# Performance work log

Measured on AMD Instinct MI355X. Metric: run time of the kernel, lower is better.

Reference implementation:

```python
import jax, jax.numpy as jnp
from jax import lax
import numpy as np

B, H, W = 16, 512, 512
OPENING_R, EROSION_R, DILATION_R = 5, 2, 1
MIN_SIZE, AREA_THRESHOLD = 2000, 300
INF = np.int32(2 ** 30)


def _disk(r):
    # skimage.morphology.disk: x^2 + y^2 <= r^2 on a (2r+1)^2 grid
    y, x = np.mgrid[-r:r + 1, -r:r + 1]
    return jnp.asarray((x * x + y * y <= r * r).astype(np.float32))


D_OPEN, D_ERODE, D_DILATE = _disk(OPENING_R), _disk(EROSION_R), _disk(DILATION_R)


def _conv2(x, k):
    return lax.conv_general_dilated(x[None, None], k[None, None], (1, 1), 'VALID')[0, 0]


def _erode(fg, se):
    # skimage binary_erosion uses border_value=True (image border does not erode)
    r = se.shape[0] // 2
    x = jnp.pad(fg.astype(jnp.float32), r, constant_values=1.0)
    return _conv2(x, se) >= se.sum() - 0.5


def _dilate(fg, se):
    # skimage binary_dilation uses border_value=False
    r = se.shape[0] // 2
    x = jnp.pad(fg.astype(jnp.float32), r, constant_values=0.0)
    return _conv2(x, se) > 0.5


def _seg_cummin(v, reset, axis, reverse):
    # segmented cumulative-min: scan resets wherever `reset` is True (background)
    def comb(a, b):
        av, af = a
        bv, bf = b
        return jnp.where(bf, bv, jnp.minimum(av, bv)), af | bf

    vv, _ = lax.associative_scan(comb, (v, reset), axis=axis, reverse=reverse)
    return vv


def _label(fg):
    # 4-connectivity connected-component labeling via min-label propagation.
    # Each fg pixel starts with its raveled index; alternating row/col segmented
    # cummin sweeps run under while_loop until a fixed point (root id per comp).
    h, w = fg.shape
    idx = jnp.arange(h * w, dtype=jnp.int32).reshape(h, w)
    lab0 = jnp.where(fg, idx, INF)
    bg = ~fg

    def sweep(l):
        for axis in (1, 0):
            for rev in (False, True):
                l = jnp.where(fg, _seg_cummin(l, bg, axis, rev), INF)
        return l

    def body(c):
        l, _ = c
        nl = sweep(l)
        return nl, jnp.array_equal(nl, l)

    lab, _ = lax.while_loop(lambda c: ~c[1], body, (lab0, jnp.array(False)))
    seg = jnp.where(fg, lab, 0).ravel()
    sizes = jax.ops.segment_sum(fg.astype(jnp.int32).ravel(), seg, num_segments=h * w)
    ncomp = jnp.sum(sizes > 0)
    return lab, sizes, ncomp


def _remove_small_objects(fg, min_size, guard):
    lab, sizes, ncomp = _label(fg)
    px = sizes[jnp.where(fg, lab, 0)]  # component size at every fg pixel
    kept = fg & (px >= min_size)
    # original only removes small objects when label(...).max() > 1
    return jnp.where(ncomp > 1, kept, fg) if guard else kept


def _pipeline(mask):
    fg = mask > 0
    fg = _remove_small_objects(fg, MIN_SIZE, True)
    # remove_small_holes == ~remove_small_objects(~fg, area_threshold + 1)
    fg = ~_remove_small_objects(~fg, AREA_THRESHOLD + 1, False)
    fg = _erode(fg, D_ERODE)
    fg = _dilate(_erode(fg, D_OPEN), D_OPEN)  # binary_opening
    fg = _remove_small_objects(fg, MIN_SIZE, True)
    fg = _dilate(fg, D_DILATE)
    return fg.astype(jnp.float32)  # original casts to int; float32 kept for vjp parity


def setup_inputs() -> dict:
    key = jax.random.key(0)
    # blobby binary masks: threshold bilinearly-upsampled low-res noise so that
    # realistic large connected components (> min_size px) exist
    low = jax.random.uniform(key, (B, H // 16, W // 16), dtype=jnp.float32)
    blob = jax.image.resize(low, (B, H, W), method='bilinear')
    return {'inputs': (blob > 0.5).astype(jnp.float32)}


def reference(inputs):
    return jax.vmap(_pipeline)(inputs)
```

## Files before the change

### kernel.cpp

```cpp
#include <hip/hip_runtime.h>
#include <stdint.h>

#define BATCH 16
#define H 512
#define W 512
#define HW (H * W)
#define NTOT (BATCH * HW)
#define NWORDS (NTOT / 64)

#define TPB 256
#define NBLK ((NTOT + TPB - 1) / TPB)
#define NBLKW ((NWORDS + TPB - 1) / TPB)

#define SROWS 16
#define SWORDS 128
#define SPIX 8192
#define NSTRIPS (NWORDS / SWORDS)

__device__ __forceinline__ int find_root_c(int* L, int x) {
    int r = x, p = L[r];
    while (p != r) { r = p; p = L[r]; }
    if (L[x] != r) atomicMin(&L[x], r);
    return r;
}

__device__ void merge_uf(int* L, int a, int b) {
    while (true) {
        a = find_root_c(L, a);
        b = find_root_c(L, b);
        if (a == b) return;
        int lo = a < b ? a : b;
        int hi = a < b ? b : a;
        int old = atomicMin(&L[hi], lo);
        if (old == hi) return;
        a = lo; b = old;
    }
}

__device__ __forceinline__ int find_root_lds(int* P, int x) {
    int r = x, p = P[r];
    while (p != r) { r = p; p = P[r]; }
    return r;
}

__device__ void merge_lds(int* P, int a, int b) {
    while (true) {
        a = find_root_lds(P, a);
        b = find_root_lds(P, b);
        if (a == b) return;
        int lo = a < b ? a : b;
        int hi = a < b ? b : a;
        int old = atomicMin(&P[hi], lo);
        if (old == hi) return;
        a = lo; b = old;
    }
}

__device__ __forceinline__ int start_of(uint64_t m, int i, int cv, int base) {
    uint64_t below = i ? ((~m) & ((1ull << i) - 1)) : 0ull;
    if (below == 0) return (cv >= 0) ? cv : base;
    int hz = 63 - __builtin_clzll(below);
    return base + hz + 1;
}

__device__ uint64_t fill_word(const uint64_t* __restrict__ bits,
                              const int* __restrict__ carry, const int* __restrict__ L,
                              const int* __restrict__ sizes, int minsz, int gw) {
    uint64_t fg = bits[gw];
    uint64_t bg = ~fg;
    uint64_t res = fg;
    int cv = carry[gw];
    int base = gw << 6;
    while (bg) {
        int s = __builtin_ctzll(bg);
        uint64_t rest = bg >> s;
        uint64_t nr = ~rest;
        int len = nr ? __builtin_ctzll(nr) : (64 - s);
        uint64_t piece = ((len >= 64) ? ~0ull : ((1ull << len) - 1)) << s;
        int start = (s == 0 && cv >= 0) ? cv : (base + s);
        if (sizes[L[start]] < minsz) res |= piece;
        bg &= ~piece;
    }
    return res;
}

template <int R, bool ERODE>
__device__ uint64_t morph_word_lds(const uint64_t* buf, int lrow, int w, int gyTop) {
    const uint64_t BORDER = ERODE ? ~0ull : 0ull;
    uint64_t res = ERODE ? ~0ull : 0ull;
#pragma unroll
    for (int dy = -R; dy <= R; ++dy) {
        int lr = lrow + dy;
        int gy = gyTop + lr;
        if (gy < 0 || gy >= H) continue;
        int v = R * R - dy * dy;
        int kx = 0;
        while ((kx + 1) * (kx + 1) <= v) ++kx;
        uint64_t cur = buf[lr * 8 + w];
        uint64_t prv = (w > 0) ? buf[lr * 8 + w - 1] : BORDER;
        uint64_t nxt = (w < 7) ? buf[lr * 8 + w + 1] : BORDER;
        uint64_t acc = cur;
#pragma unroll
        for (int dx = 1; dx <= kx; ++dx) {
            uint64_t right = (cur >> dx) | (nxt << (64 - dx));
            uint64_t left  = (cur << dx) | (prv >> (64 - dx));
            if (ERODE) acc &= right & left;
            else       acc |= right | left;
        }
        if (ERODE) res &= acc;
        else       res |= acc;
    }
    return res;
}

__global__ void k_thresh_pack(const float* __restrict__ in, uint64_t* __restrict__ bits) {
    int p = blockIdx.x * blockDim.x + threadIdx.x;
    bool a = (p < NTOT) && (in[p] > 0.0f);
    uint64_t b = __ballot(a);
    if ((threadIdx.x & 63) == 0 && p < NTOT) bits[p >> 6] = b;
}

__global__ void k_strip_ccl(const uint64_t* __restrict__ bits, int inv,
                            int* __restrict__ carry, int* __restrict__ L,
                            int* __restrict__ sizes, int* __restrict__ ncomp) {
    __shared__ uint64_t sw[SWORDS];
    __shared__ int scarry[SWORDS];
    __shared__ int par[SPIX];
    int blk = blockIdx.x;
    int t = threadIdx.x;
    uint64_t inv64 = inv ? ~0ull : 0ull;
    uint64_t m = bits[blk * SWORDS + t] ^ inv64;
    sw[t] = m;
    __syncthreads();

    if (t < SROWS) {
        int cv = -1;
        for (int i = 0; i < 8; ++i) {
            int lw = t * 8 + i;
            scarry[lw] = cv;
            uint64_t w = sw[lw];
            if (w >> 63) {
                uint64_t z = ~w;
                if (z == 0) { if (cv < 0) cv = lw << 6; }
                else { int hz = 63 - __builtin_clzll(z); cv = (lw << 6) + hz + 1; }
            } else cv = -1;
        }
    }
    __syncthreads();

    int cv = scarry[t];
    carry[blk * SWORDS + t] = (cv >= 0) ? (blk * SPIX + cv) : -1;
    int lbase = t << 6;
    uint64_t starts = m & ~((m << 1) | ((cv >= 0) ? 1ull : 0ull));
    uint64_t ss = starts;
    while (ss) {
        int s = __builtin_ctzll(ss);
        par[lbase + s] = lbase + s;
        ss &= ss - 1;
    }
    __syncthreads();

    if (t >= 8 && m) {
        uint64_t up = sw[t - 8];
        uint64_t cand = m & up;
        if (cand) {
            uint64_t curprev = (t & 7) ? sw[t - 1] : 0ull;
            uint64_t upprev  = (t & 7) ? sw[t - 9] : 0ull;
            uint64_t curl = (m << 1) | (curprev >> 63);
            uint64_t upl  = (up << 1) | (upprev >> 63);
            cand &= ~(curl & upl);
            int cvu = scarry[t - 8];
            while (cand) {
                int i = __builtin_ctzll(cand);
                int sP = start_of(m, i, cv, lbase);
                int sQ = start_of(up, i, cvu, lbase - 512);
                merge_lds(par, sP, sQ);
                cand &= cand - 1;
            }
        }
    }
    __syncthreads();

    int gpix = blk * SPIX;
    ss = starts;
    while (ss) {
        int s = __builtin_ctzll(ss);
        int ls = lbase + s;
        int r = find_root_lds(par, ls);
        L[gpix + ls] = gpix + r;
        if (r == ls) sizes[gpix + ls] = 0;
        ss &= ss - 1;
    }
    if (t == 0 && (blk & 31) == 0) ncomp[blk >> 5] = 0;
}

__global__ void k_merge_bound(const uint64_t* __restrict__ bits, int inv,
                              const int* __restrict__ carry, int* __restrict__ L) {
    int tid = threadIdx.x;
    if (tid >= 248) return;
    int img = blockIdx.x;
    int y = ((tid >> 3) + 1) * SROWS;
    int w = tid & 7;
    int gw = img * 4096 + y * 8 + w;
    uint64_t inv64 = inv ? ~0ull : 0ull;
    uint64_t cur = bits[gw] ^ inv64;
    uint64_t up  = bits[gw - 8] ^ inv64;
    uint64_t cand = cur & up;
    if (!cand) return;
    uint64_t curprev = w ? (bits[gw - 1] ^ inv64) : 0ull;
    uint64_t upprev  = w ? (bits[gw - 9] ^ inv64) : 0ull;
    uint64_t curl = (cur << 1) | (curprev >> 63);
    uint64_t upl  = (up << 1)  | (upprev >> 63);
    cand &= ~(curl & upl);
    if (!cand) return;
    int cvc = carry[gw], cvu = carry[gw - 8];
    int base = gw << 6;
    while (cand) {
        int i = __builtin_ctzll(cand);
        int sP = start_of(cur, i, cvc, base);
        int sQ = start_of(up, i, cvu, base - W);
        merge_uf(L, sP, sQ);
        cand &= cand - 1;
    }
}

__global__ void k_flatten_count(const uint64_t* __restrict__ bits, int inv,
                                const int* __restrict__ carry, int* __restrict__ L,
                                int* __restrict__ sizes, int* __restrict__ ncomp) {
    __shared__ int hk[128];
    __shared__ int hv[128];
    for (int i = threadIdx.x; i < 128; i += TPB) { hk[i] = -1; hv[i] = 0; }
    __syncthreads();

    int gw = blockIdx.x * blockDim.x + threadIdx.x;
    if (gw < NWORDS) {
        uint64_t inv64 = inv ? ~0ull : 0ull;
        uint64_t m = bits[gw] ^ inv64;
        if (m) {
            int cv = carry[gw];
            int base = gw << 6;
            while (m) {
                int s = __builtin_ctzll(m);
                uint64_t rest = m >> s;
                uint64_t nr = ~rest;
                int len = nr ? __builtin_ctzll(nr) : (64 - s);
                uint64_t piece = ((len >= 64) ? ~0ull : ((1ull << len) - 1)) << s;
                bool initial = !(s == 0 && cv >= 0);
                int start = initial ? (base + s) : cv;
                int r = find_root_c(L, start);
                if (initial && r == start) atomicAdd(&ncomp[gw >> 12], 1);
                int cnt = __popcll(piece);
                uint32_t h = ((uint32_t)r * 2654435761u) >> 25;
                bool done = false;
                for (int tt = 0; tt < 16; ++tt) {
                    int slot = (h + tt) & 127;
                    int k = hk[slot];
                    if (k == -1) k = atomicCAS(&hk[slot], -1, r);
                    if (k == -1 || k == r) { atomicAdd(&hv[slot], cnt); done = true; break; }
                }
                if (!done) atomicAdd(&sizes[r], cnt);
                m &= ~piece;
            }
        }
    }
    __syncthreads();
    for (int i = threadIdx.x; i < 128; i += TPB)
        if (hk[i] != -1) atomicAdd(&sizes[hk[i]], hv[i]);
}

__global__ void k_keep_guard(const uint64_t* __restrict__ bits,
                             const int* __restrict__ carry, const int* __restrict__ L,
                             const int* __restrict__ sizes, const int* __restrict__ ncomp,
                             int minsz, uint64_t* __restrict__ out) {
    int gw = blockIdx.x * blockDim.x + threadIdx.x;
    if (gw >= NWORDS) return;
    uint64_t m = bits[gw];
    uint64_t res = m;
    if (m && ncomp[gw >> 12] > 1) {
        int cv = carry[gw];
        int base = gw << 6;
        while (m) {
            int s = __builtin_ctzll(m);
            uint64_t rest = m >> s;
            uint64_t nr = ~rest;
            int len = nr ? __builtin_ctzll(nr) : (64 - s);
            uint64_t piece = ((len >= 64) ? ~0ull : ((1ull << len) - 1)) << s;
            int start = (s == 0 && cv >= 0) ? cv : (base + s);
            if (sizes[L[start]] < minsz) res &= ~piece;
            m &= ~piece;
        }
    }
    out[gw] = res;
}

__global__ void k_fill_morph(const uint64_t* __restrict__ bits,
                             const int* __restrict__ carry, const int* __restrict__ L,
                             const int* __restrict__ sizes,
                             uint64_t* __restrict__ out) {
    __shared__ uint64_t bufA[56 * 8];
    __shared__ uint64_t bufB[56 * 8];
    int img = blockIdx.x >> 4;
    int s   = blockIdx.x & 15;
    int y0 = s * 32;
    int gyTop = y0 - 12;
    int t = threadIdx.x;

    for (int lw = t; lw < 56 * 8; lw += TPB) {
        int gy = gyTop + (lw >> 3);
        int w = lw & 7;
        uint64_t v = 0;
        if (gy >= 0 && gy < H)
            v = fill_word(bits, carry, L, sizes, 301, img * 4096 + gy * 8 + w);
        bufA[lw] = v;
    }
    __syncthreads();

    for (int lw = t; lw < 56 * 8; lw += TPB) {
        int lr = lw >> 3;
        if (lr < 2 || lr > 53) continue;
        bufB[lw] = morph_word_lds<2, true>(bufA, lr, lw & 7, gyTop);
    }
    __syncthreads();

    for (int lw = t; lw < 56 * 8; lw += TPB) {
        int lr = lw >> 3;
        if (lr < 7 || lr > 48) continue;
        bufA[lw] = morph_word_lds<5, true>(bufB, lr, lw & 7, gyTop);
    }
    __syncthreads();

    for (int lw = t; lw < 56 * 8; lw += TPB) {
        int lr = lw >> 3;
        if (lr < 12 || lr > 43) continue;
        uint64_t v = morph_word_lds<5, false>(bufA, lr, lw & 7, gyTop);
        int gy = gyTop + lr;
        out[img * 4096 + gy * 8 + (lw & 7)] = v;
    }
}

__global__ void k_to_float_dilate(const uint64_t* __restrict__ bits,
                                  float* __restrict__ out) {
    int p = blockIdx.x * blockDim.x + threadIdx.x;
    if (p >= NTOT) return;
    int gw = p >> 6;
    int i = p & 63;
    int w = gw & 7;
    int y = (gw >> 3) & (H - 1);
    uint64_t cur = bits[gw];
    uint64_t up  = (y > 0)     ? bits[gw - 8] : 0ull;
    uint64_t dn  = (y < H - 1) ? bits[gw + 8] : 0ull;
    uint64_t prv = (w > 0)     ? bits[gw - 1] : 0ull;
    uint64_t nxt = (w < 7)     ? bits[gw + 1] : 0ull;
    uint64_t d = cur | up | dn | (cur << 1) | (prv >> 63) | (cur >> 1) | (nxt << 63);
    out[p] = ((d >> i) & 1ull) ? 1.0f : 0.0f;
}

extern "C" void kernel_launch(void* const* d_in, const int* in_sizes, int n_in,
                              void* d_out, int out_size, void* d_ws, size_t ws_size,
                              hipStream_t stream) {
    const float* in = (const float*)d_in[0];
    float* out = (float*)d_out;

    uint8_t* ws = (uint8_t*)d_ws;
    int* labels = (int*)ws;
    int* sizes  = (int*)(ws + (size_t)NTOT * 4);
    uint64_t* bitsA = (uint64_t*)(ws + (size_t)NTOT * 8);
    uint64_t* bitsB = bitsA + NWORDS;
    int* carry = (int*)(bitsB + NWORDS);
    int* ncomp = carry + NWORDS;

    k_thresh_pack<<<NBLK, TPB, 0, stream>>>(in, bitsA);

    k_strip_ccl<<<NSTRIPS, SWORDS, 0, stream>>>(bitsA, 0, carry, labels, sizes, ncomp);
    k_merge_bound<<<BATCH, 256, 0, stream>>>(bitsA, 0, carry, labels);
    k_flatten_count<<<NBLKW, TPB, 0, stream>>>(bitsA, 0, carry, labels, sizes, ncomp);
    k_keep_guard<<<NBLKW, TPB, 0, stream>>>(bitsA, carry, labels, sizes, ncomp, 2000, bitsB);

    k_strip_ccl<<<NSTRIPS, SWORDS, 0, stream>>>(bitsB, 1, carry, labels, sizes, ncomp);
    k_merge_bound<<<BATCH, 256, 0, stream>>>(bitsB, 1, carry, labels);
    k_flatten_count<<<NBLKW, TPB, 0, stream>>>(bitsB, 1, carry, labels, sizes, ncomp);

    k_fill_morph<<<BATCH * 16, TPB, 0, stream>>>(bitsB, carry, labels, sizes, bitsA);

    k_strip_ccl<<<NSTRIPS, SWORDS, 0, stream>>>(bitsA, 0, carry, labels, sizes, ncomp);
    k_merge_bound<<<BATCH, 256, 0, stream>>>(bitsA, 0, carry, labels);
    k_flatten_count<<<NBLKW, TPB, 0, stream>>>(bitsA, 0, carry, labels, sizes, ncomp);
    k_keep_guard<<<NBLKW, TPB, 0, stream>>>(bitsA, carry, labels, sizes, ncomp, 2000, bitsB);

    k_to_float_dilate<<<NBLK, TPB, 0, stream>>>(bitsB, out);
}
```

Measured before the change: 212.6 us.

## Fuse keep-guard into next strip CCL and into final dilate/float output

```diff
diff --git a/kernel.cpp b/kernel.cpp
--- a/kernel.cpp
+++ b/kernel.cpp
@@ -61,6 +61,29 @@
     if (below == 0) return (cv >= 0) ? cv : base;
     int hz = 63 - __builtin_clzll(below);
     return base + hz + 1;
+}
+
+__device__ uint64_t keep_word(const uint64_t* __restrict__ bits,
+                              const int* __restrict__ carry, const int* __restrict__ L,
+                              const int* __restrict__ sizes, const int* __restrict__ ncomp,
+                              int minsz, int gw) {
+    uint64_t m = bits[gw];
+    uint64_t res = m;
+    if (m && ncomp[gw >> 12] > 1) {
+        int cv = carry[gw];
+        int base = gw << 6;
+        while (m) {
+            int s = __builtin_ctzll(m);
+            uint64_t rest = m >> s;
+            uint64_t nr = ~rest;
+            int len = nr ? __builtin_ctzll(nr) : (64 - s);
+            uint64_t piece = ((len >= 64) ? ~0ull : ((1ull << len) - 1)) << s;
+            int start = (s == 0 && cv >= 0) ? cv : (base + s);
+            if (sizes[L[start]] < minsz) res &= ~piece;
+            m &= ~piece;
+        }
+    }
+    return res;
 }
 
 __device__ uint64_t fill_word(const uint64_t* __restrict__ bits,
@@ -113,23 +136,10 @@
     return res;
 }
 
-__global__ void k_thresh_pack(const float* __restrict__ in, uint64_t* __restrict__ bits) {
-    int p = blockIdx.x * blockDim.x + threadIdx.x;
-    bool a = (p < NTOT) && (in[p] > 0.0f);
-    uint64_t b = __ballot(a);
-    if ((threadIdx.x & 63) == 0 && p < NTOT) bits[p >> 6] = b;
-}
-
-__global__ void k_strip_ccl(const uint64_t* __restrict__ bits, int inv,
-                            int* __restrict__ carry, int* __restrict__ L,
-                            int* __restrict__ sizes, int* __restrict__ ncomp) {
-    __shared__ uint64_t sw[SWORDS];
-    __shared__ int scarry[SWORDS];
-    __shared__ int par[SPIX];
-    int blk = blockIdx.x;
-    int t = threadIdx.x;
-    uint64_t inv64 = inv ? ~0ull : 0ull;
-    uint64_t m = bits[blk * SWORDS + t] ^ inv64;
+__device__ void strip_ccl_body(uint64_t m, uint64_t* sw, int* scarry, int* par,
+                               int blk, int t,
+                               int* __restrict__ carry, int* __restrict__ L,
+                               int* __restrict__ sizes, int* __restrict__ ncomp) {
     sw[t] = m;
     __syncthreads();
 
@@ -192,6 +202,43 @@
         ss &= ss - 1;
     }
     if (t == 0 && (blk & 31) == 0) ncomp[blk >> 5] = 0;
+}
+
+__global__ void k_thresh_pack(const float* __restrict__ in, uint64_t* __restrict__ bits) {
+    int p = blockIdx.x * blockDim.x + threadIdx.x;
+    bool a = (p < NTOT) && (in[p] > 0.0f);
+    uint64_t b = __ballot(a);
+    if ((threadIdx.x & 63) == 0 && p < NTOT) bits[p >> 6] = b;
+}
+
+__global__ void k_strip_ccl(const uint64_t* __restrict__ bits, int inv,
+                            int* __restrict__ carry, int* __restrict__ L,
+                            int* __restrict__ sizes, int* __restrict__ ncomp) {
+    __shared__ uint64_t sw[SWORDS];
+    __shared__ int scarry[SWORDS];
+    __shared__ int par[SPIX];
+    int blk = blockIdx.x;
+    int t = threadIdx.x;
+    uint64_t inv64 = inv ? ~0ull : 0ull;
+    uint64_t m = bits[blk * SWORDS + t] ^ inv64;
+    strip_ccl_body(m, sw, scarry, par, blk, t, carry, L, sizes, ncomp);
+}
+
+__global__ void k_keep_strip(const uint64_t* __restrict__ bits,
+                             const int* __restrict__ carryIn, const int* __restrict__ Lin,
+                             const int* __restrict__ sizesIn, const int* __restrict__ ncompIn,
+                             uint64_t* __restrict__ outBits,
+                             int* __restrict__ carryOut, int* __restrict__ Lout,
+                             int* __restrict__ sizesOut, int* __restrict__ ncompOut) {
+    __shared__ uint64_t sw[SWORDS];
+    __shared__ int scarry[SWORDS];
+    __shared__ int par[SPIX];
+    int blk = blockIdx.x;
+    int t = threadIdx.x;
+    int gw = blk * SWORDS + t;
+    uint64_t kw = keep_word(bits, carryIn, Lin, sizesIn, ncompIn, 2000, gw);
+    outBits[gw] = kw;
+    strip_ccl_body(~kw, sw, scarry, par, blk, t, carryOut, Lout, sizesOut, ncompOut);
 }
 
 __global__ void k_merge_bound(const uint64_t* __restrict__ bits, int inv,
@@ -268,31 +315,6 @@
         if (hk[i] != -1) atomicAdd(&sizes[hk[i]], hv[i]);
 }
 
-__global__ void k_keep_guard(const uint64_t* __restrict__ bits,
-                             const int* __restrict__ carry, const int* __restrict__ L,
-                             const int* __restrict__ sizes, const int* __restrict__ ncomp,
-                             int minsz, uint64_t* __restrict__ out) {
-    int gw = blockIdx.x * blockDim.x + threadIdx.x;
-    if (gw >= NWORDS) return;
-    uint64_t m = bits[gw];
-    uint64_t res = m;
-    if (m && ncomp[gw >> 12] > 1) {
-        int cv = carry[gw];
-        int base = gw << 6;
-        while (m) {
-            int s = __builtin_ctzll(m);
-            uint64_t rest = m >> s;
-            uint64_t nr = ~rest;
-            int len = nr ? __builtin_ctzll(nr) : (64 - s);
-            uint64_t piece = ((len >= 64) ? ~0ull : ((1ull << len) - 1)) << s;
-            int start = (s == 0 && cv >= 0) ? cv : (base + s);
-            if (sizes[L[start]] < minsz) res &= ~piece;
-            m &= ~piece;
-        }
-    }
-    out[gw] = res;
-}
-
 __global__ void k_fill_morph(const uint64_t* __restrict__ bits,
                              const int* __restrict__ carry, const int* __restrict__ L,
                              const int* __restrict__ sizes,
@@ -338,21 +360,53 @@
     }
 }
 
-__global__ void k_to_float_dilate(const uint64_t* __restrict__ bits,
-                                  float* __restrict__ out) {
-    int p = blockIdx.x * blockDim.x + threadIdx.x;
-    if (p >= NTOT) return;
-    int gw = p >> 6;
-    int i = p & 63;
-    int w = gw & 7;
-    int y = (gw >> 3) & (H - 1);
-    uint64_t cur = bits[gw];
-    uint64_t up  = (y > 0)     ? bits[gw - 8] : 0ull;
-    uint64_t dn  = (y < H - 1) ? bits[gw + 8] : 0ull;
-    uint64_t prv = (w > 0)     ? bits[gw - 1] : 0ull;
-    uint64_t nxt = (w < 7)     ? bits[gw + 1] : 0ull;
-    uint64_t d = cur | up | dn | (cur << 1) | (prv >> 63) | (cur >> 1) | (nxt << 63);
-    out[p] = ((d >> i) & 1ull) ? 1.0f : 0.0f;
+__global__ void k_keep_dilate_float(const uint64_t* __restrict__ bits,
+                                    const int* __restrict__ carry, const int* __restrict__ L,
+                                    const int* __restrict__ sizes, const int* __restrict__ ncomp,
+                                    float* __restrict__ out) {
+    __shared__ uint64_t kb[10 * 8];
+    __shared__ uint64_t db[8 * 8];
+    int blk = blockIdx.x;
+    int img = blk >> 6;
+    int s = blk & 63;
+    int y0 = s * 8;
+    int t = threadIdx.x;
+
+    if (t < 80) {
+        int lr = t >> 3;
+        int w = t & 7;
+        int gy = y0 - 1 + lr;
+        uint64_t v = 0;
+        if (gy >= 0 && gy < H)
+            v = keep_word(bits, carry, L, sizes, ncomp, 2000, img * 4096 + gy * 8 + w);
+        kb[t] = v;
+    }
+    __syncthreads();
+    if (t < 64) {
+        int r = t >> 3, w = t & 7;
+        uint64_t cur = kb[(r + 1) * 8 + w];
+        uint64_t up  = kb[r * 8 + w];
+        uint64_t dn  = kb[(r + 2) * 8 + w];
+        uint64_t prv = w ? kb[(r + 1) * 8 + w - 1] : 0ull;
+        uint64_t nxt = (w < 7) ? kb[(r + 1) * 8 + w + 1] : 0ull;
+        db[t] = cur | up | dn | (cur << 1) | (prv >> 63) | (cur >> 1) | (nxt << 63);
+    }
+    __syncthreads();
+
+    int q0 = t * 16;
+    uint64_t wd = db[q0 >> 6];
+    int sh = q0 & 63;
+    float4* o = (float4*)(out + (size_t)img * HW + (size_t)y0 * W + q0);
+#pragma unroll
+    for (int k = 0; k < 4; ++k) {
+        uint32_t nib = (uint32_t)(wd >> (sh + k * 4)) & 0xFu;
+        float4 f;
+        f.x = (nib & 1u) ? 1.0f : 0.0f;
+        f.y = (nib & 2u) ? 1.0f : 0.0f;
+        f.z = (nib & 4u) ? 1.0f : 0.0f;
+        f.w = (nib & 8u) ? 1.0f : 0.0f;
+        o[k] = f;
+    }
 }
 
 extern "C" void kernel_launch(void* const* d_in, const int* in_sizes, int n_in,
@@ -362,30 +416,34 @@
     float* out = (float*)d_out;
 
     uint8_t* ws = (uint8_t*)d_ws;
-    int* labels = (int*)ws;
-    int* sizes  = (int*)(ws + (size_t)NTOT * 4);
-    uint64_t* bitsA = (uint64_t*)(ws + (size_t)NTOT * 8);
+    int* LA      = (int*)ws;
+    int* sizesA  = (int*)(ws + (size_t)NTOT * 4);
+    int* LB      = (int*)(ws + (size_t)NTOT * 8);
+    int* sizesB  = (int*)(ws + (size_t)NTOT * 12);
+    uint64_t* bitsA = (uint64_t*)(ws + (size_t)NTOT * 16);
     uint64_t* bitsB = bitsA + NWORDS;
-    int* carry = (int*)(bitsB + NWORDS);
-    int* ncomp = carry + NWORDS;
+    uint64_t* bits3 = bitsB + NWORDS;
+    int* carryA = (int*)(bits3 + NWORDS);
+    int* carryB = carryA + NWORDS;
+    int* ncompA = carryB + NWORDS;
+    int* ncompB = ncompA + BATCH;
 
     k_thresh_pack<<<NBLK, TPB, 0, stream>>>(in, bitsA);
 
-    k_strip_ccl<<<NSTRIPS, SWORDS, 0, stream>>>(bitsA, 0, carry, labels, sizes, ncomp);
-    k_merge_bound<<<BATCH, 256, 0, stream>>>(bitsA, 0, carry, labels);
-    k_flatten_count<<<NBLKW, TPB, 0, stream>>>(bitsA, 0, carry, labels, sizes, ncomp);
-    k_keep_guard<<<NBLKW, TPB, 0, stream>>>(bitsA, carry, labels, sizes, ncomp, 2000, bitsB);
-
-    k_strip_ccl<<<NSTRIPS, SWORDS, 0, stream>>>(bitsB, 1, carry, labels, sizes, ncomp);
-    k_merge_bound<<<BATCH, 256, 0, stream>>>(bitsB, 1, carry, labels);
-    k_flatten_count<<<NBLKW, TPB, 0, stream>>>(bitsB, 1, carry, labels, sizes, ncomp);
-
-    k_fill_morph<<<BATCH * 16, TPB, 0, stream>>>(bitsB, carry, labels, sizes, bitsA);
-
-    k_strip_ccl<<<NSTRIPS, SWORDS, 0, stream>>>(bitsA, 0, carry, labels, sizes, ncomp);
-    k_merge_bound<<<BATCH, 256, 0, stream>>>(bitsA, 0, carry, labels);
-    k_flatten_count<<<NBLKW, TPB, 0, stream>>>(bitsA, 0, carry, labels, sizes, ncomp);
-    k_keep_guard<<<NBLKW, TPB, 0, stream>>>(bitsA, carry, labels, sizes, ncomp, 2000, bitsB);
-
-    k_to_float_dilate<<<NBLK, TPB, 0, stream>>>(bitsB, out);
-}
+    k_strip_ccl<<<NSTRIPS, SWORDS, 0, stream>>>(bitsA, 0, carryA, LA, sizesA, ncompA);
+    k_merge_bound<<<BATCH, 256, 0, stream>>>(bitsA, 0, carryA, LA);
+    k_flatten_count<<<NBLKW, TPB, 0, stream>>>(bitsA, 0, carryA, LA, sizesA, ncompA);
+
+    k_keep_strip<<<NSTRIPS, SWORDS, 0, stream>>>(bitsA, carryA, LA, sizesA, ncompA,
+                                                 bitsB, carryB, LB, sizesB, ncompB);
+    k_merge_bound<<<BATCH, 256, 0, stream>>>(bitsB, 1, carryB, LB);
+    k_flatten_count<<<NBLKW, TPB, 0, stream>>>(bitsB, 1, carryB, LB, sizesB, ncompB);
+
+    k_fill_morph<<<BATCH * 16, TPB, 0, stream>>>(bitsB, carryB, LB, sizesB, bits3);
+
+    k_strip_ccl<<<NSTRIPS, SWORDS, 0, stream>>>(bits3, 0, carryA, LA, sizesA, ncompA);
+    k_merge_bound<<<BATCH, 256, 0, stream>>>(bits3, 0, carryA, LA);
+    k_flatten_count<<<NBLKW, TPB, 0, stream>>>(bits3, 0, carryA, LA, sizesA, ncompA);
+
+    k_keep_dilate_float<<<BATCH * 64, TPB, 0, stream>>>(bits3, carryA, LA, sizesA, ncompA, out);
+}
```

New measurement: 204.0 us. 1.04x faster.
